# Kernel tuning notes

Measured on AMD Instinct MI355X. Metric: run time of the kernel, lower is better.

## Reference

```python
import jax, jax.numpy as jnp
import numpy as np

B, V, C = 256, 50, 40
VOCAB, D, H, NH, T = 10000, 256, 256, 8, 1000


def setup_inputs():
    key = jax.random.key(0)
    ks = jax.random.split(key, 24)
    f = lambda k, shape, s=0.05: jax.random.normal(k, shape, jnp.float32) * s
    # nn.Embedding(vocab_size+1, d_model, padding_idx=-1): last row is the padding row (zeros)
    emb = f(ks[0], (VOCAB + 1, D), 0.1).at[VOCAB].set(0.0)
    return dict(
        input_seqs=jax.random.randint(ks[1], (B, V, C), 0, VOCAB),
        seq_time_step=jax.random.uniform(ks[2], (B, V), jnp.float32, 0.0, 365.0),
        diffusion_time_t=jax.random.randint(ks[3], (B,), 0, T),
        normal_noise=jax.random.normal(ks[4], (B, V, D), jnp.float32),
        predicted_noise=jax.random.normal(ks[5], (B, V, D), jnp.float32),
        emb=emb,
        betas=jnp.asarray(np.linspace(1e-4, 0.02, T, dtype=np.float32)),
        tl_w=f(ks[6], (64, 1), 0.5), tl_b=f(ks[7], (64,), 0.1),
        tu_w=f(ks[8], (D, 64)), tu_b=f(ks[9], (D,), 0.01),
        in_proj_w=f(ks[10], (3 * D, D)), in_proj_b=f(ks[11], (3 * D,), 0.01),
        out_proj_w=f(ks[12], (D, D)), out_proj_b=f(ks[13], (D,), 0.01),
        w_ih=f(ks[14], (4 * H, D)), w_hh=f(ks[15], (4 * H, H)),
        b_ih=f(ks[16], (4 * H,), 0.01), b_hh=f(ks[17], (4 * H,), 0.01),
        c1_w=f(ks[18], (4 * H, H)), c1_b=f(ks[19], (4 * H,), 0.01),
        c2_w=f(ks[20], (4 * H, 4 * H)), c2_b=f(ks[21], (4 * H,), 0.01),
        co_w=f(ks[22], (2, 4 * H)), co_b=f(ks[23], (2,), 0.01),
    )


def _mha(q, kv, wi, bi, wo, bo):
    # torch MultiheadAttention on 2-D inputs -> unbatched; 'sequence length' = batch dim B
    hd = D // NH
    qp = (q @ wi[:D].T + bi[:D]).reshape(-1, NH, hd)
    kp = (kv @ wi[D:2 * D].T + bi[D:2 * D]).reshape(-1, NH, hd)
    vp = (kv @ wi[2 * D:].T + bi[2 * D:]).reshape(-1, NH, hd)
    s = jnp.einsum('qhd,khd->hqk', qp, kp) * (hd ** -0.5)
    o = jnp.einsum('hqk,khd->qhd', jax.nn.softmax(s, -1), vp).reshape(-1, D)
    return o @ wo.T + bo


def _lstm_final(seq, w_ih, w_hh, b_ih, b_hh):
    # unbatched nn.LSTM over the batch axis (length B). The original's try-branch always
    # raises (seq_h squeezed to 1-D), so the zero-init except-branch runs every visit.
    xg = seq @ w_ih.T + (b_ih + b_hh)  # [B, 4H]
    def step(carry, x):
        h, c = carry
        i, fg, g, o = jnp.split(x + h @ w_hh.T, 4)
        c = jax.nn.sigmoid(fg) * c + jax.nn.sigmoid(i) * jnp.tanh(g)
        h = jax.nn.sigmoid(o) * jnp.tanh(c)
        return (h, c), None
    z = jnp.zeros((H,), seq.dtype)
    (h, _), _ = jax.lax.scan(step, (z, z), xg)
    return h  # [H]


def _classify(h, w1, b1, w2, b2, wo, bo):
    h = jax.nn.relu(h @ w1.T + b1)
    h = jax.nn.relu(h @ w2.T + b2)
    return jax.nn.softmax(h @ wo.T + bo, -1)


def reference(input_seqs, seq_time_step, diffusion_time_t, normal_noise, predicted_noise,
              emb, betas, tl_w, tl_b, tu_w, tu_b, in_proj_w, in_proj_b, out_proj_w,
              out_proj_b, w_ih, w_hh, b_ih, b_hh, c1_w, c1_b, c2_w, c2_b, co_w, co_b):
    tt = seq_time_step[..., None] / 180.0
    tenc = (1.0 - jnp.tanh((tt @ tl_w.T + tl_b) ** 2)) @ tu_w.T + tu_b  # [B,V,D]
    ve = jax.nn.relu(emb[input_seqs]).sum(-2) + tenc                     # [B,V,D]
    alpha = jnp.cumprod(1.0 - betas)[diffusion_time_t][:, None, None]
    ven = ve * jnp.sqrt(alpha) + normal_noise * jnp.sqrt(1.0 - alpha)
    gen1 = ve + (ven - predicted_noise)
    # gen2 recurrence: row i = MHA(row i-1, gen1[:,i], gen1[:,i]); row -1 is the
    # vocab_size-filled initial tensor (valid negative index, try never fails).
    def att_step(prev, kv):
        out = _mha(prev, kv, in_proj_w, in_proj_b, out_proj_w, out_proj_b)
        return out, out
    _, gen2 = jax.lax.scan(att_step, jnp.full((B, D), float(VOCAB), ve.dtype),
                           gen1.transpose(1, 0, 2))                    # [V,B,D]
    lstm = lambda s: _lstm_final(s, w_ih, w_hh, b_ih, b_hh)
    hv = jax.vmap(lstm)(ve.transpose(1, 0, 2))  # [V,H]
    hg = jax.vmap(lstm)(gen2)                   # [V,H]
    res = jnp.broadcast_to(_classify(hv, c1_w, c1_b, c2_w, c2_b, co_w, co_b)[None], (B, V, 2))
    resg = jnp.broadcast_to(_classify(hg, c1_w, c1_b, c2_w, c2_b, co_w, co_b)[None], (B, V, 2))
    return (res, resg, res[:, -1], resg[:, -1], normal_noise, predicted_noise)
```

## Files before the change

### kernel.cpp

```cpp
#include <hip/hip_runtime.h>

#define BB 256
#define VV 50
#define CC 40
#define DD 256
#define HH 256
#define NHH 8
#define TT 1000

typedef unsigned short u16;
typedef unsigned int u32;
typedef _Float16 h2v __attribute__((ext_vector_type(2)));

__device__ __forceinline__ float blf(u16 x){ union{u32 u; float f;} z; z.u=(u32)x<<16; return z.f; }
__device__ __forceinline__ float ld(const void* p, long i, int f){
  if(f) return ((const float*)p)[i];
  return blf(((const u16*)p)[i]);
}
__device__ __forceinline__ u32 packh2(float a, float b){
  union { h2v h; u32 u; } z;
  z.h = h2v{(_Float16)a, (_Float16)b};
  return z.u;
}
__device__ __forceinline__ float fdot2(u32 a, u32 b, float c){
#if __has_builtin(__builtin_amdgcn_fdot2)
  union { u32 u; h2v h; } x, y; x.u=a; y.u=b;
  return __builtin_amdgcn_fdot2(x.h, y.h, c, false);
#else
  union { u32 u; _Float16 h[2]; } x, y; x.u=a; y.u=b;
  return c + (float)x.h[0]*(float)y.h[0] + (float)x.h[1]*(float)y.h[1];
#endif
}
__device__ __forceinline__ float sigm(float x){ return 1.f/(1.f+__expf(-x)); }
__device__ __forceinline__ float tanh_fast(float x){ return 1.f - 2.f/(__expf(2.f*x)+1.f); }

__global__ void k_flag(const void* betas, int* flag){
  if(threadIdx.x==0) flag[0] = (((const u32*)betas)[0] == 0x38D1B717u) ? 1 : 0;
}

__global__ void k_prep(const void* betas, const int* fl, float* sqa, float* s1a){
  __shared__ float sp[256];
  int t = threadIdx.x;
  int f = fl[0];
  float om[4]; float p = 1.f;
  #pragma unroll
  for(int k=0;k<4;k++){ int i=t*4+k; float be=(i<TT)?ld(betas,i,f):0.f; om[k]=1.f-be; p*=om[k]; }
  sp[t]=p; __syncthreads();
  for(int off=1; off<256; off<<=1){
    float x = (t>=off) ? sp[t-off]*sp[t] : sp[t];
    __syncthreads(); sp[t]=x; __syncthreads();
  }
  float c = (t>0)? sp[t-1] : 1.f;
  #pragma unroll
  for(int k=0;k<4;k++){
    c *= om[k]; int i=t*4+k;
    if(i<TT){ sqa[i]=sqrtf(c); s1a[i]=sqrtf(fmaxf(1.f-c,0.f)); }
  }
}

__global__ void k_packT(const void* src, float* dst, int N, int K, long elemoff, const int* fl){
  int i = blockIdx.x*256 + threadIdx.x;
  int tot = N*(K>>2);
  if(i>=tot) return;
  int f = fl[0];
  int d4 = i / N, j = i - d4*N;
  long o = elemoff + (long)j*K + (d4<<2);
  float4 r; r.x=ld(src,o,f); r.y=ld(src,o+1,f); r.z=ld(src,o+2,f); r.w=ld(src,o+3,f);
  ((float4*)dst)[i] = r;
}

__global__ void k_packQO(const void* src, u32* dst, long elemoff, const int* fl){
  int i = blockIdx.x*256 + threadIdx.x;
  if(i >= 32768) return;
  int f = fl[0];
  int c2 = i >> 8, j = i & 255;
  float a = ld(src, elemoff + (long)j*256 + 2*c2,     f);
  float b = ld(src, elemoff + (long)j*256 + 2*c2 + 1, f);
  dst[(c2>>2)*1024 + j*4 + (c2&3)] = packh2(a,b);
}

__global__ void k_packH(const void* src, u32* dst, int N, int K, const int* fl){
  int i = blockIdx.x*256 + threadIdx.x;
  int tot = N*(K>>1);
  if(i >= tot) return;
  int f = fl[0];
  int c2 = i / N, j = i - c2*N;
  float a = ld(src, (long)j*K + 2*c2,     f);
  float b = ld(src, (long)j*K + 2*c2 + 1, f);
  dst[(c2>>2)*(N*4) + j*4 + (c2&3)] = packh2(a,b);
}

__global__ void k_packW2(const void* src, u32* whhR, u32* wclQ, const int* fl){
  int i = blockIdx.x*256 + threadIdx.x;
  if(i >= 131072) return;
  int f = fl[0];
  int row = i >> 7, cp = i & 127;
  float a = ld(src, (long)row*256 + 2*cp,     f);
  float b = ld(src, (long)row*256 + 2*cp + 1, f);
  u32 v = packh2(a,b);
  int q = cp >> 5, pp = cp & 31;
  int rb = row & 127, m = row >> 7;
  int j = q*128 + rb;
  if(pp < 24){
    int idx = m*24 + pp;
    whhR[(idx>>2)*2048 + j*4 + (idx&3)] = v;
  } else {
    int h = (pp-24) >> 2, e = (pp-24) & 3;
    wclQ[((m*2+h)*512 + j)*4 + e] = v;
  }
}

__global__ void k_ve_gen1(const int* seqs, const void* sts, const int* dt,
    const void* nn, const void* pn, const void* emb, const void* tl_w, const void* tl_b,
    const float* tu4, const void* tu_b, const float* sqa, const float* s1a, const int* fl,
    float* ve, float* gen1){
  int bv = blockIdx.x; int b = bv / VV;
  int t = threadIdx.x;
  int f = fl[0];
  __shared__ float4 f4[16];
  __shared__ int idx[CC];
  float tt = ld(sts,bv,f) * (1.f/180.f);
  if(t<64){ float x = tt*ld(tl_w,t,f) + ld(tl_b,t,f); ((float*)f4)[t] = 1.f - tanhf(x*x); }
  if(t<CC) idx[t] = seqs[bv*CC+t];
  __syncthreads();
  float acc = ld(tu_b,t,f);
  const float4* tu = (const float4*)tu4;
  #pragma unroll
  for(int d4=0; d4<16; d4++){
    float4 w = tu[d4*DD + t];
    float4 fv = f4[d4];
    acc += fv.x*w.x+fv.y*w.y+fv.z*w.z+fv.w*w.w;
  }
  float s=0.f;
  for(int c=0;c<CC;c++){ float e = ld(emb,(long)idx[c]*DD + t,f); s += fmaxf(e,0.f); }
  float vev = s + acc;
  ve[bv*DD+t] = vev;
  int tb = dt[b];
  float sa=sqa[tb], s1=s1a[tb];
  gen1[bv*DD+t] = vev*(1.f+sa) + ld(nn,(long)bv*DD+t,f)*s1 - ld(pn,(long)bv*DD+t,f);
}

__global__ void k_copy(const void* nn, const void* pn, const int* fl, float* out){
  int i = blockIdx.x*256 + threadIdx.x;
  int f = fl[0];
  const int n = BB*VV*DD;
  if(i<n){ out[52224+i]=ld(nn,i,f); out[52224+n+i]=ld(pn,i,f); }
}

__global__ void k_kvproj(const float* gen1, const u32* wkP, const u32* wvP,
                         const void* bi, const int* fl, u32* kpHq, u32* vp){
  int g = blockIdx.x; int v = g>>4; int b0 = (g&15)<<4;
  int t = threadIdx.x;
  int f = fl[0];
  __shared__ __align__(16) u32 xp[16][128];
  for(int r=0;r<16;r++){
    float xv = gen1[((b0+r)*VV + v)*DD + t];
    float xb = __shfl_xor(xv, 1, 64);
    if((t&1)==0) xp[r][t>>1] = packh2(xv, xb);
  }
  __syncthreads();
  float ak[16], av[16];
  float bk = ld(bi,DD+t,f), bvv = ld(bi,2*DD+t,f);
  #pragma unroll
  for(int r=0;r<16;r++){ ak[r]=bk; av[r]=bvv; }
  const uint4* wk4 = (const uint4*)wkP;
  const uint4* wv4 = (const uint4*)wvP;
  for(int c8=0;c8<32;c8++){
    uint4 kk = wk4[c8*256+t], vv = wv4[c8*256+t];
    #pragma unroll
    for(int r=0;r<16;r++){
      uint4 xx = ((const uint4*)xp[r])[c8];
      ak[r] = fdot2(xx.x, kk.x, ak[r]); ak[r] = fdot2(xx.y, kk.y, ak[r]);
      ak[r] = fdot2(xx.z, kk.z, ak[r]); ak[r] = fdot2(xx.w, kk.w, ak[r]);
      av[r] = fdot2(xx.x, vv.x, av[r]); av[r] = fdot2(xx.y, vv.y, av[r]);
      av[r] = fdot2(xx.z, vv.z, av[r]); av[r] = fdot2(xx.w, vv.w, av[r]);
    }
  }
  #pragma unroll
  for(int r=0;r<16;r++){
    float a2 = __shfl_xor(ak[r], 1, 64);
    if((t&1)==0)
      kpHq[(size_t)v*32768 + (t>>3)*1024 + (size_t)(b0+r)*4 + ((t>>1)&3)] = packh2(ak[r], a2);
  }
  #pragma unroll
  for(int i2=0;i2<8;i2++){
    int k2 = (b0>>1) + i2;
    vp[(size_t)v*32768 + (k2>>2)*1024 + t*4 + (k2&3)] = packh2(av[2*i2], av[2*i2+1]);
  }
}

__global__ __launch_bounds__(256) void k_mha_all(const u32* kpHq, const u32* vp,
    const u32* wqp, const u32* wop, const void* ipb, const void* opb, const int* fl,
    float* gen2){
  int i = blockIdx.x, t = threadIdx.x;
  int f = fl[0];
  __shared__ __align__(16) u32 kls[32768];
  __shared__ __align__(16) u32 xp[128];
  __shared__ __align__(16) u32 qpp[128];
  __shared__ float s[NHH][257];
  __shared__ __align__(16) u32 sp[NHH][128];
  __shared__ __align__(16) u32 op[128];
  __shared__ float mh[NHH], rs[NHH];
  float bq = ld(ipb, t, f);
  float bo = ld(opb, t, f);
  if(t < 128) xp[t] = packh2(10000.f, 10000.f);
  __syncthreads();
  const uint4* xp4 = (const uint4*)xp;
  const uint4* op4 = (const uint4*)op;
  const uint4* wq4p = (const uint4*)wqp;
  const uint4* wo4p = (const uint4*)wop;
  const uint4* kls4 = (const uint4*)kls;
  const uint4* qp4  = (const uint4*)qpp;
  int hg = t>>5, ln = t&31;
  for(int v=0; v<VV; v++){
    {
      const u32* kg = kpHq + (size_t)v*32768;
#if __has_builtin(__builtin_amdgcn_global_load_lds)
      #pragma unroll
      for(int j=0;j<32;j++){
        __builtin_amdgcn_global_load_lds(
          (const __attribute__((address_space(1))) u32*)(kg + (j*256 + t)*4),
          (__attribute__((address_space(3))) u32*)(kls + (j*256 + t)*4), 16, 0, 0);
      }
#else
      const uint4* kg4 = (const uint4*)kg;
      uint4* kl4 = (uint4*)kls;
      #pragma unroll 8
      for(int j=0;j<32;j++) kl4[j*256+t] = kg4[j*256+t];
#endif
    }
    {
      float acc = bq;
      #pragma unroll 8
      for(int c8=0;c8<32;c8++){
        uint4 xx = xp4[c8];
        uint4 ww = wq4p[c8*256 + t];
        acc = fdot2(xx.x, ww.x, acc); acc = fdot2(xx.y, ww.y, acc);
        acc = fdot2(xx.z, ww.z, acc); acc = fdot2(xx.w, ww.w, acc);
      }
      float aq2 = __shfl_xor(acc, 1, 64);
      if((t&1)==0) qpp[t>>1] = packh2(acc, aq2);
    }
    asm volatile("s_waitcnt vmcnt(0)" ::: "memory");
    __syncthreads();
    {
      #pragma unroll
      for(int h=0; h<NHH; h++){
        float acc = 0.f;
        #pragma unroll
        for(int dd=0; dd<4; dd++){
          uint4 kk = kls4[(h*4+dd)*256 + t];
          uint4 qq = qp4[h*4+dd];
          acc = fdot2(qq.x, kk.x, acc); acc = fdot2(qq.y, kk.y, acc);
          acc = fdot2(qq.z, kk.z, acc); acc = fdot2(qq.w, kk.w, acc);
        }
        s[h][t] = acc*0.1767766952966369f;
      }
    }
    __syncthreads();
    float m=-3.0e38f;
    for(int k=ln;k<BB;k+=32) m=fmaxf(m, s[hg][k]);
    for(int off=16;off;off>>=1) m=fmaxf(m, __shfl_down(m,off,32));
    if(ln==0) mh[hg]=m;
    __syncthreads();
    #pragma unroll
    for(int h=0;h<NHH;h++) s[h][t]=__expf(s[h][t]-mh[h]);
    __syncthreads();
    float sm=0.f;
    for(int k=ln;k<BB;k+=32) sm += s[hg][k];
    for(int off=16;off;off>>=1) sm += __shfl_down(sm,off,32);
    if(ln==0) rs[hg]=1.f/sm;
    #pragma unroll
    for(int m2=t; m2<1024; m2+=256){
      int h = m2>>7, k2 = m2&127;
      sp[h][k2] = packh2(s[h][2*k2], s[h][2*k2+1]);
    }
    __syncthreads();
    {
      const uint4* vb = (const uint4*)(vp + (size_t)v*32768);
      const uint4* spv = (const uint4*)sp[hg];
      float acc = 0.f;
      #pragma unroll 8
      for(int k8=0;k8<32;k8++){
        uint4 pv = spv[k8];
        uint4 vv = vb[k8*256 + t];
        acc = fdot2(pv.x, vv.x, acc); acc = fdot2(pv.y, vv.y, acc);
        acc = fdot2(pv.z, vv.z, acc); acc = fdot2(pv.w, vv.w, acc);
      }
      float o = acc * rs[hg];
      float oo = __shfl_xor(o, 1, 64);
      if((t&1)==0) op[t>>1] = packh2(o, oo);
    }
    __syncthreads();
    {
      float acc = bo;
      #pragma unroll 8
      for(int c8=0;c8<32;c8++){
        uint4 xx = op4[c8];
        uint4 ww = wo4p[c8*256 + t];
        acc = fdot2(xx.x, ww.x, acc); acc = fdot2(xx.y, ww.y, acc);
        acc = fdot2(xx.z, ww.z, acc); acc = fdot2(xx.w, ww.w, acc);
      }
      gen2[((size_t)v*BB+i)*DD + t] = acc;
      float ax = __shfl_xor(acc, 1, 64);
      if((t&1)==0) xp[t>>1] = packh2(acc, ax);
    }
    __syncthreads();
  }
}

__global__ __launch_bounds__(256, 2) void k_xg(const float* inp, int is_ve, const u32* wihP,
                     const void* b_ih, const void* b_hh, const int* fl, u16* xg){
  int g = blockIdx.x; int v=g>>4; int b0=(g&15)<<4;
  int t = threadIdx.x;
  int f = fl[0];
  __shared__ __align__(16) u32 xp[16][128];
  for(int r=0;r<16;r++){
    int b = b0+r;
    const float* src = is_ve ? (inp + (b*VV+v)*DD) : (inp + (v*BB+b)*DD);
    float xv = src[t];
    float xb = __shfl_xor(xv, 1, 64);
    if((t&1)==0) xp[r][t>>1] = packh2(xv, xb);
  }
  __syncthreads();
  float acc[4][16];
  #pragma unroll
  for(int js=0;js<4;js++){
    float bsum = ld(b_ih,js*256+t,f) + ld(b_hh,js*256+t,f);
    #pragma unroll
    for(int r=0;r<16;r++) acc[js][r]=bsum;
  }
  const uint4* wp4 = (const uint4*)wihP;
  for(int c8=0; c8<32; c8++){
    uint4 w[4];
    #pragma unroll
    for(int js=0;js<4;js++) w[js] = wp4[c8*1024 + js*256 + t];
    #pragma unroll
    for(int r=0;r<16;r++){
      uint4 xx = ((const uint4*)xp[r])[c8];
      #pragma unroll
      for(int js=0;js<4;js++){
        acc[js][r] = fdot2(xx.x, w[js].x, acc[js][r]);
        acc[js][r] = fdot2(xx.y, w[js].y, acc[js][r]);
        acc[js][r] = fdot2(xx.z, w[js].z, acc[js][r]);
        acc[js][r] = fdot2(xx.w, w[js].w, acc[js][r]);
      }
    }
  }
  for(int r=0;r<16;r++)
    #pragma unroll
    for(int js=0;js<4;js++){
      union { _Float16 h; u16 u; } z;
      z.h = (_Float16)acc[js][r];
      xg[(size_t)(v*BB + b0 + r)*1024 + js*256 + t] = z.u;
    }
}

__global__ __attribute__((amdgpu_flat_work_group_size(512,512)))
__attribute__((amdgpu_waves_per_eu(2,2)))
void k_lstm3(const u16* xgA, const u16* xgB,
    const u32* whhR, const u32* wclQ, float* hfin){
  int b = blockIdx.x, j = threadIdx.x;
  int q = j >> 7, rb = j & 127;
  const u16* xgv = (b < VV) ? (xgA + (size_t)b*BB*1024) : (xgB + (size_t)(b-VV)*BB*1024);
  __shared__ __align__(16) u32 wcl[32768];
  __shared__ __align__(16) float pacc[4][1024];
  __shared__ __align__(16) u32 hp[128];
  u32 w[192];
  { const uint4* wr4 = (const uint4*)whhR;
    #pragma unroll
    for(int i4=0;i4<48;i4++){
      uint4 v = wr4[i4*512 + j];
      w[i4*4+0]=v.x; w[i4*4+1]=v.y; w[i4*4+2]=v.z; w[i4*4+3]=v.w;
    } }
  {
    const uint4* src = (const uint4*)wclQ;
    uint4* dst = (uint4*)wcl;
    #pragma unroll
    for(int i=0;i<16;i++) dst[i*512 + j] = src[i*512 + j];
  }
  if(j < 128) hp[j] = 0u;
  float c0 = 0.f, h_t = 0.f;
  __syncthreads();
  const uint4* hp4 = (const uint4*)hp;
  const uint4* wcl4 = (const uint4*)wcl;
  for(int s=0; s<BB; s++){
    asm volatile("" ::: "memory");
    u16 nx0=0,nx1=0,nx2=0,nx3=0;
    if(j < 256){
      nx0 = xgv[s*1024 +       j];
      nx1 = xgv[s*1024 + 256 + j];
      nx2 = xgv[s*1024 + 512 + j];
      nx3 = xgv[s*1024 + 768 + j];
    }
    float acc[8];
    #pragma unroll
    for(int m=0;m<8;m++) acc[m]=0.f;
    #pragma unroll
    for(int i=0;i<6;i++){
      uint4 hh = hp4[q*8 + i];
      #pragma unroll
      for(int m=0;m<8;m++){
        acc[m] = fdot2(hh.x, w[m*24 + i*4+0], acc[m]);
        acc[m] = fdot2(hh.y, w[m*24 + i*4+1], acc[m]);
        acc[m] = fdot2(hh.z, w[m*24 + i*4+2], acc[m]);
        acc[m] = fdot2(hh.w, w[m*24 + i*4+3], acc[m]);
      }
    }
    #pragma unroll
    for(int h=0;h<2;h++){
      uint4 hh = hp4[q*8 + 6 + h];
      #pragma unroll
      for(int m=0;m<8;m++){
        uint4 s4 = wcl4[(m*2+h)*512 + j];
        acc[m] = fdot2(hh.x, s4.x, acc[m]);
        acc[m] = fdot2(hh.y, s4.y, acc[m]);
        acc[m] = fdot2(hh.z, s4.z, acc[m]);
        acc[m] = fdot2(hh.w, s4.w, acc[m]);
      }
    }
    #pragma unroll
    for(int m=0;m<8;m++) pacc[q][m*128 + rb] = acc[m];
    __syncthreads();
    if(j < 256){
      float a0 = pacc[0][      j] + pacc[1][      j] + pacc[2][      j] + pacc[3][      j];
      float a1 = pacc[0][256 + j] + pacc[1][256 + j] + pacc[2][256 + j] + pacc[3][256 + j];
      float a2 = pacc[0][512 + j] + pacc[1][512 + j] + pacc[2][512 + j] + pacc[3][512 + j];
      float a3 = pacc[0][768 + j] + pacc[1][768 + j] + pacc[2][768 + j] + pacc[3][768 + j];
      float ai = a0 + (float)(*(const _Float16*)&nx0);
      float af = a1 + (float)(*(const _Float16*)&nx1);
      float ag = a2 + (float)(*(const _Float16*)&nx2);
      float ao = a3 + (float)(*(const _Float16*)&nx3);
      float ig = sigm(ai), fg = sigm(af), og = sigm(ao);
      float gg = tanh_fast(ag);
      c0 = fg*c0 + ig*gg;
      h_t = og*tanh_fast(c0);
      float ho = __shfl_xor(h_t, 1, 64);
      if((j&1)==0) hp[j>>1] = packh2(h_t, ho);
    }
    __syncthreads();
  }
  if(j < 256) hfin[b*HH + j] = h_t;
}

__global__ void k_cls(const float* hfin, const u32* c1p, const void* c1b,
                      const u32* c2p, const void* c2b, const void* cow, const void* cob,
                      const int* fl, float* cls){
  int blk = blockIdx.x;
  int t = threadIdx.x;
  int f = fl[0];
  __shared__ __align__(16) u32 hp1[128];
  __shared__ __align__(16) u32 h2p[512];
  __shared__ float h24[1024];
  __shared__ float red0[4], red1[4];
  {
    float hv = hfin[blk*HH + t];
    float hb = __shfl_xor(hv, 1, 64);
    if((t&1)==0) hp1[t>>1] = packh2(hv, hb);
  }
  __syncthreads();
  const uint4* hp14 = (const uint4*)hp1;
  const uint4* c1p4 = (const uint4*)c1p;
  {
    float a[4];
    #pragma unroll
    for(int js=0;js<4;js++) a[js]=ld(c1b,js*256+t,f);
    #pragma unroll 8
    for(int c8=0;c8<32;c8++){
      uint4 hh = hp14[c8];
      #pragma unroll
      for(int js=0;js<4;js++){
        uint4 ww = c1p4[c8*1024 + js*256+t];
        a[js] = fdot2(hh.x, ww.x, a[js]); a[js] = fdot2(hh.y, ww.y, a[js]);
        a[js] = fdot2(hh.z, ww.z, a[js]); a[js] = fdot2(hh.w, ww.w, a[js]);
      }
    }
    #pragma unroll
    for(int js=0;js<4;js++){
      float v = fmaxf(a[js],0.f);
      float vb = __shfl_xor(v, 1, 64);
      if((t&1)==0) h2p[(js*256+t)>>1] = packh2(v, vb);
    }
  }
  __syncthreads();
  const uint4* h2p4 = (const uint4*)h2p;
  const uint4* c2p4 = (const uint4*)c2p;
  {
    float a[4];
    #pragma unroll
    for(int js=0;js<4;js++) a[js]=ld(c2b,js*256+t,f);
    #pragma unroll 8
    for(int c8=0;c8<128;c8++){
      uint4 hh = h2p4[c8];
      #pragma unroll
      for(int js=0;js<4;js++){
        uint4 ww = c2p4[c8*1024 + js*256+t];
        a[js] = fdot2(hh.x, ww.x, a[js]); a[js] = fdot2(hh.y, ww.y, a[js]);
        a[js] = fdot2(hh.z, ww.z, a[js]); a[js] = fdot2(hh.w, ww.w, a[js]);
      }
    }
    #pragma unroll
    for(int js=0;js<4;js++) h24[js*256+t] = fmaxf(a[js],0.f);
  }
  __syncthreads();
  float p0=0.f,p1=0.f;
  #pragma unroll
  for(int js=0;js<4;js++){
    int j=js*256+t;
    float hv=h24[j];
    p0 += hv*ld(cow,j,f);
    p1 += hv*ld(cow,1024+j,f);
  }
  for(int off=32;off;off>>=1){ p0+=__shfl_down(p0,off,64); p1+=__shfl_down(p1,off,64); }
  if((t&63)==0){ red0[t>>6]=p0; red1[t>>6]=p1; }
  __syncthreads();
  if(t==0){
    float l0 = ld(cob,0,f) + red0[0]+red0[1]+red0[2]+red0[3];
    float l1 = ld(cob,1,f) + red1[0]+red1[1]+red1[2]+red1[3];
    float mm = fmaxf(l0,l1);
    float e0=__expf(l0-mm), e1=__expf(l1-mm);
    float inv = 1.f/(e0+e1);
    cls[blk*2] = e0*inv; cls[blk*2+1] = e1*inv;
  }
}

__global__ void k_out(const float* cls, float* out){
  int i = blockIdx.x*256 + threadIdx.x;
  if(i < BB*VV*2){
    int v = (i>>1) % VV, k = i&1;
    out[i] = cls[v*2+k];
    out[BB*VV*2 + i] = cls[(VV+v)*2+k];
  }
  if(i < BB*2){
    int k=i&1;
    out[2*BB*VV*2 + i]        = cls[(VV-1)*2+k];
    out[2*BB*VV*2 + BB*2 + i] = cls[(2*VV-1)*2+k];
  }
}

extern "C" void kernel_launch(void* const* d_in, const int* in_sizes, int n_in,
                              void* d_out, int out_size, void* d_ws, size_t ws_size,
                              hipStream_t stream){
  const int* seqs = (const int*)d_in[0];
  const void* sts  = d_in[1];
  const int* dt   = (const int*)d_in[2];
  const void* nn   = d_in[3];
  const void* pn   = d_in[4];
  const void* emb  = d_in[5];
  const void* betas= d_in[6];
  const void* tl_w = d_in[7];
  const void* tl_b = d_in[8];
  const void* tu_w = d_in[9];
  const void* tu_b = d_in[10];
  const void* ipw  = d_in[11];
  const void* ipb  = d_in[12];
  const void* opw  = d_in[13];
  const void* opb  = d_in[14];
  const void* wih  = d_in[15];
  const void* whh  = d_in[16];
  const void* bih  = d_in[17];
  const void* bhh  = d_in[18];
  const void* c1w  = d_in[19];
  const void* c1b  = d_in[20];
  const void* c2w  = d_in[21];
  const void* c2b  = d_in[22];
  const void* cow  = d_in[23];
  const void* cob  = d_in[24];

  char* base = (char*)d_ws;
  u32*   wkP  = (u32*)(base + 0);
  u32*   wvP  = (u32*)(base + 131072);
  u32*   wqp  = (u32*)(base + 524288);
  u32*   wop  = (u32*)(base + 655360);
  u32*   wihP = (u32*)(base + 786432);
  u32*   whhR = (u32*)(base + 1835008);
  u32*   wclQ = (u32*)(base + 2228224);
  u32*   c1p  = (u32*)(base + 2359296);
  u32*   c2p  = (u32*)(base + 3407872);
  float* tu4  = (float*)(base + 7602176);
  float* sqa  = (float*)(base + 7667712);
  float* s1a  = (float*)(base + 7671808);
  float* hfin = (float*)(base + 7675904);
  float* cls  = (float*)(base + 7778304);
  int*   flag = (int*)(base + 7779328);
  float* ve   = (float*)(base + 7783424);
  float* g12  = (float*)(base + 20890624);
  char*  arena= base + 33997824;
  u32*   kpHq = (u32*)(arena);
  u32*   vp   = (u32*)(arena + 13107200);
  u16*   xgA  = (u16*)(arena);
  u16*   xgB  = (u16*)(arena + 26214400);
  float* out  = (float*)d_out;

  k_flag<<<1,64,0,stream>>>(betas, flag);
  k_prep<<<1,256,0,stream>>>(betas, flag, sqa, s1a);
  k_packQO<<<128,256,0,stream>>>(ipw, wkP, 65536L,  flag);
  k_packQO<<<128,256,0,stream>>>(ipw, wvP, 131072L, flag);
  k_packQO<<<128,256,0,stream>>>(ipw, wqp, 0, flag);
  k_packQO<<<128,256,0,stream>>>(opw, wop, 0, flag);
  k_packH<<<512,256,0,stream>>>(wih, wihP, 1024, 256, flag);
  k_packW2<<<512,256,0,stream>>>(whh, whhR, wclQ, flag);
  k_packH<<<512,256,0,stream>>>(c1w, c1p, 1024, 256, flag);
  k_packH<<<2048,256,0,stream>>>(c2w, c2p, 1024, 1024, flag);
  k_packT<<<16,256,0,stream>>>(tu_w, tu4, 256, 64, 0, flag);

  k_ve_gen1<<<BB*VV,256,0,stream>>>(seqs,sts,dt,nn,pn,emb,tl_w,tl_b,tu4,tu_b,sqa,s1a,flag,ve,g12);
  k_copy<<<(BB*VV*DD+255)/256,256,0,stream>>>(nn,pn,flag,out);

  k_kvproj<<<VV*16,256,0,stream>>>(g12, wkP, wvP, ipb, flag, kpHq, vp);
  k_mha_all<<<BB,256,0,stream>>>(kpHq, vp, wqp, wop, ipb, opb, flag, g12);

  k_xg<<<VV*16,256,0,stream>>>(ve,  1, wihP, bih, bhh, flag, xgA);
  k_xg<<<VV*16,256,0,stream>>>(g12, 0, wihP, bih, bhh, flag, xgB);
  k_lstm3<<<100,512,0,stream>>>(xgA, xgB, whhR, wclQ, hfin);

  k_cls<<<2*VV,256,0,stream>>>(hfin, c1p, c1b, c2p, c2b, cow, cob, flag, cls);
  k_out<<<100,256,0,stream>>>(cls, out);
}
```

Measured before the change: 1.563 ms.

## Fuse weight-pack kernels into one launch and use shuffle reductions in LSTM

All the flag, prep and weight-packing kernels are merged into a single mega-kernel that dispatches on block index, so eleven small launches become one. The LSTM recurrence is restructured so that each wave owns 16 hidden rows across the four K-quarters. Partial sums are then reduced with cross-lane shuffles instead of a shared-memory pacc array and a second barrier. The hidden state is double-buffered so only one __syncthreads per timestep remains, and the whh packing layout is changed to match the new thread mapping.

```diff
diff --git a/kernel.cpp b/kernel.cpp
--- a/kernel.cpp
+++ b/kernel.cpp
@@ -34,14 +34,9 @@
 __device__ __forceinline__ float sigm(float x){ return 1.f/(1.f+__expf(-x)); }
 __device__ __forceinline__ float tanh_fast(float x){ return 1.f - 2.f/(__expf(2.f*x)+1.f); }
 
-__global__ void k_flag(const void* betas, int* flag){
-  if(threadIdx.x==0) flag[0] = (((const u32*)betas)[0] == 0x38D1B717u) ? 1 : 0;
-}
-
-__global__ void k_prep(const void* betas, const int* fl, float* sqa, float* s1a){
-  __shared__ float sp[256];
-  int t = threadIdx.x;
-  int f = fl[0];
+
+__device__ __forceinline__ void prep_body(const void* betas, int f, int t,
+                                          float* sqa, float* s1a, float* sp){
   float om[4]; float p = 1.f;
   #pragma unroll
   for(int k=0;k<4;k++){ int i=t*4+k; float be=(i<TT)?ld(betas,i,f):0.f; om[k]=1.f-be; p*=om[k]; }
@@ -58,49 +53,50 @@
   }
 }
 
-__global__ void k_packT(const void* src, float* dst, int N, int K, long elemoff, const int* fl){
-  int i = blockIdx.x*256 + threadIdx.x;
-  int tot = N*(K>>2);
-  if(i>=tot) return;
-  int f = fl[0];
-  int d4 = i / N, j = i - d4*N;
-  long o = elemoff + (long)j*K + (d4<<2);
-  float4 r; r.x=ld(src,o,f); r.y=ld(src,o+1,f); r.z=ld(src,o+2,f); r.w=ld(src,o+3,f);
-  ((float4*)dst)[i] = r;
-}
-
-__global__ void k_packQO(const void* src, u32* dst, long elemoff, const int* fl){
-  int i = blockIdx.x*256 + threadIdx.x;
+__device__ __forceinline__ void packQO_body(const void* src, u32* dst, long elemoff,
+                                            int f, int lb, int t){
+  int i = lb*256 + t;
   if(i >= 32768) return;
-  int f = fl[0];
   int c2 = i >> 8, j = i & 255;
   float a = ld(src, elemoff + (long)j*256 + 2*c2,     f);
   float b = ld(src, elemoff + (long)j*256 + 2*c2 + 1, f);
   dst[(c2>>2)*1024 + j*4 + (c2&3)] = packh2(a,b);
 }
 
-__global__ void k_packH(const void* src, u32* dst, int N, int K, const int* fl){
-  int i = blockIdx.x*256 + threadIdx.x;
+__device__ __forceinline__ void packH_body(const void* src, u32* dst, int N, int K,
+                                           int f, int lb, int t){
+  int i = lb*256 + t;
   int tot = N*(K>>1);
   if(i >= tot) return;
-  int f = fl[0];
   int c2 = i / N, j = i - c2*N;
   float a = ld(src, (long)j*K + 2*c2,     f);
   float b = ld(src, (long)j*K + 2*c2 + 1, f);
   dst[(c2>>2)*(N*4) + j*4 + (c2&3)] = packh2(a,b);
 }
 
-__global__ void k_packW2(const void* src, u32* whhR, u32* wclQ, const int* fl){
-  int i = blockIdx.x*256 + threadIdx.x;
+__device__ __forceinline__ void packT_body(const void* src, float* dst, int N, int K,
+                                           int f, int lb, int t){
+  int i = lb*256 + t;
+  int tot = N*(K>>2);
+  if(i>=tot) return;
+  int d4 = i / N, j = i - d4*N;
+  long o = (long)j*K + (d4<<2);
+  float4 r; r.x=ld(src,o,f); r.y=ld(src,o+1,f); r.z=ld(src,o+2,f); r.w=ld(src,o+3,f);
+  ((float4*)dst)[i] = r;
+}
+
+__device__ __forceinline__ void packW2_body(const void* src, u32* whhR, u32* wclQ,
+                                            int f, int lb, int t){
+  int i = lb*256 + t;
   if(i >= 131072) return;
-  int f = fl[0];
   int row = i >> 7, cp = i & 127;
   float a = ld(src, (long)row*256 + 2*cp,     f);
   float b = ld(src, (long)row*256 + 2*cp + 1, f);
   u32 v = packh2(a,b);
   int q = cp >> 5, pp = cp & 31;
-  int rb = row & 127, m = row >> 7;
-  int j = q*128 + rb;
+  int m = row >> 7, rsB = row & 127;
+  int w = rsB >> 4, li = rsB & 15;
+  int j = w*64 + q*16 + li;
   if(pp < 24){
     int idx = m*24 + pp;
     whhR[(idx>>2)*2048 + j*4 + (idx&3)] = v;
@@ -108,6 +104,29 @@
     int h = (pp-24) >> 2, e = (pp-24) & 3;
     wclQ[((m*2+h)*512 + j)*4 + e] = v;
   }
+}
+
+__global__ void k_mega(const void* betas, const void* ipw, const void* opw,
+    const void* wih, const void* whh, const void* c1w, const void* c2w, const void* tu_w,
+    int* flag, float* sqa, float* s1a,
+    u32* wkP, u32* wvP, u32* wqp, u32* wop, u32* wihP,
+    u32* whhR, u32* wclQ, u32* c1p, u32* c2p, float* tu4){
+  __shared__ float sp[256];
+  int f = (((const u32*)betas)[0] == 0x38D1B717u) ? 1 : 0;
+  int g = blockIdx.x, t = threadIdx.x;
+  if(g == 0){
+    if(t == 0) flag[0] = f;
+    prep_body(betas, f, t, sqa, s1a, sp);
+  }
+  else if(g < 129)  packQO_body(ipw, wkP, 65536L,  f, g-1,   t);
+  else if(g < 257)  packQO_body(ipw, wvP, 131072L, f, g-129, t);
+  else if(g < 385)  packQO_body(ipw, wqp, 0L,      f, g-257, t);
+  else if(g < 513)  packQO_body(opw, wop, 0L,      f, g-385, t);
+  else if(g < 1025) packH_body(wih, wihP, 1024, 256,  f, g-513,  t);
+  else if(g < 1537) packW2_body(whh, whhR, wclQ,      f, g-1025, t);
+  else if(g < 2049) packH_body(c1w, c1p, 1024, 256,   f, g-1537, t);
+  else if(g < 4097) packH_body(c2w, c2p, 1024, 1024,  f, g-2049, t);
+  else              packT_body(tu_w, tu4, 256, 64,    f, g-4097, t);
 }
 
 __global__ void k_ve_gen1(const int* seqs, const void* sts, const int* dt,
@@ -361,11 +380,12 @@
 void k_lstm3(const u16* xgA, const u16* xgB,
     const u32* whhR, const u32* wclQ, float* hfin){
   int b = blockIdx.x, j = threadIdx.x;
-  int q = j >> 7, rb = j & 127;
+  int l = j & 63;
+  int q = l >> 4, li = l & 15;
+  int rs = (j>>6)*16 + li;
   const u16* xgv = (b < VV) ? (xgA + (size_t)b*BB*1024) : (xgB + (size_t)(b-VV)*BB*1024);
   __shared__ __align__(16) u32 wcl[32768];
-  __shared__ __align__(16) float pacc[4][1024];
-  __shared__ __align__(16) u32 hp[128];
+  __shared__ __align__(16) u32 hp[2][128];
   u32 w[192];
   { const uint4* wr4 = (const uint4*)whhR;
     #pragma unroll
@@ -379,26 +399,22 @@
     #pragma unroll
     for(int i=0;i<16;i++) dst[i*512 + j] = src[i*512 + j];
   }
-  if(j < 128) hp[j] = 0u;
-  float c0 = 0.f, h_t = 0.f;
-  __syncthreads();
-  const uint4* hp4 = (const uint4*)hp;
+  if(j < 128) hp[0][j] = 0u;
+  float cA = 0.f, cB = 0.f, hA = 0.f, hB = 0.f;
+  __syncthreads();
   const uint4* wcl4 = (const uint4*)wcl;
   for(int s=0; s<BB; s++){
     asm volatile("" ::: "memory");
-    u16 nx0=0,nx1=0,nx2=0,nx3=0;
-    if(j < 256){
-      nx0 = xgv[s*1024 +       j];
-      nx1 = xgv[s*1024 + 256 + j];
-      nx2 = xgv[s*1024 + 512 + j];
-      nx3 = xgv[s*1024 + 768 + j];
-    }
+    const uint4* hc = (const uint4*)hp[s&1];
+    u16 nx[8];
+    #pragma unroll
+    for(int m=0;m<8;m++) nx[m] = xgv[s*1024 + rs + 128*m];
     float acc[8];
     #pragma unroll
     for(int m=0;m<8;m++) acc[m]=0.f;
     #pragma unroll
     for(int i=0;i<6;i++){
-      uint4 hh = hp4[q*8 + i];
+      uint4 hh = hc[q*8 + i];
       #pragma unroll
       for(int m=0;m<8;m++){
         acc[m] = fdot2(hh.x, w[m*24 + i*4+0], acc[m]);
@@ -409,7 +425,7 @@
     }
     #pragma unroll
     for(int h=0;h<2;h++){
-      uint4 hh = hp4[q*8 + 6 + h];
+      uint4 hh = hc[q*8 + 6 + h];
       #pragma unroll
       for(int m=0;m<8;m++){
         uint4 s4 = wcl4[(m*2+h)*512 + j];
@@ -420,27 +436,35 @@
       }
     }
     #pragma unroll
-    for(int m=0;m<8;m++) pacc[q][m*128 + rb] = acc[m];
-    __syncthreads();
-    if(j < 256){
-      float a0 = pacc[0][      j] + pacc[1][      j] + pacc[2][      j] + pacc[3][      j];
-      float a1 = pacc[0][256 + j] + pacc[1][256 + j] + pacc[2][256 + j] + pacc[3][256 + j];
-      float a2 = pacc[0][512 + j] + pacc[1][512 + j] + pacc[2][512 + j] + pacc[3][512 + j];
-      float a3 = pacc[0][768 + j] + pacc[1][768 + j] + pacc[2][768 + j] + pacc[3][768 + j];
-      float ai = a0 + (float)(*(const _Float16*)&nx0);
-      float af = a1 + (float)(*(const _Float16*)&nx1);
-      float ag = a2 + (float)(*(const _Float16*)&nx2);
-      float ao = a3 + (float)(*(const _Float16*)&nx3);
-      float ig = sigm(ai), fg = sigm(af), og = sigm(ao);
-      float gg = tanh_fast(ag);
-      c0 = fg*c0 + ig*gg;
-      h_t = og*tanh_fast(c0);
-      float ho = __shfl_xor(h_t, 1, 64);
-      if((j&1)==0) hp[j>>1] = packh2(h_t, ho);
-    }
-    __syncthreads();
-  }
-  if(j < 256) hfin[b*HH + j] = h_t;
+    for(int m=0;m<8;m++){
+      float a = acc[m];
+      a += __shfl_xor(a, 16, 64);
+      a += __shfl_xor(a, 32, 64);
+      acc[m] = a + (float)(*(const _Float16*)&nx[m]);
+    }
+    {
+      float igA=sigm(acc[0]), fgA=sigm(acc[2]), ogA=sigm(acc[6]);
+      float ggA=tanh_fast(acc[4]);
+      cA = fgA*cA + igA*ggA;
+      hA = ogA*tanh_fast(cA);
+      float igB=sigm(acc[1]), fgB=sigm(acc[3]), ogB=sigm(acc[7]);
+      float ggB=tanh_fast(acc[5]);
+      cB = fgB*cB + igB*ggB;
+      hB = ogB*tanh_fast(cB);
+      float hA2 = __shfl_xor(hA, 1, 64);
+      float hB2 = __shfl_xor(hB, 1, 64);
+      if(q==0 && (li&1)==0){
+        int base = (j>>6)*8 + (li>>1);
+        hp[(s+1)&1][base]      = packh2(hA, hA2);
+        hp[(s+1)&1][64 + base] = packh2(hB, hB2);
+      }
+    }
+    __syncthreads();
+  }
+  if(q==0){
+    hfin[b*HH + rs]       = hA;
+    hfin[b*HH + rs + 128] = hB;
+  }
 }
 
 __global__ void k_cls(const float* hfin, const u32* c1p, const void* c1b,
@@ -592,17 +616,8 @@
   u16*   xgB  = (u16*)(arena + 26214400);
   float* out  = (float*)d_out;
 
-  k_flag<<<1,64,0,stream>>>(betas, flag);
-  k_prep<<<1,256,0,stream>>>(betas, flag, sqa, s1a);
-  k_packQO<<<128,256,0,stream>>>(ipw, wkP, 65536L,  flag);
-  k_packQO<<<128,256,0,stream>>>(ipw, wvP, 131072L, flag);
-  k_packQO<<<128,256,0,stream>>>(ipw, wqp, 0, flag);
-  k_packQO<<<128,256,0,stream>>>(opw, wop, 0, flag);
-  k_packH<<<512,256,0,stream>>>(wih, wihP, 1024, 256, flag);
-  k_packW2<<<512,256,0,stream>>>(whh, whhR, wclQ, flag);
-  k_packH<<<512,256,0,stream>>>(c1w, c1p, 1024, 256, flag);
-  k_packH<<<2048,256,0,stream>>>(c2w, c2p, 1024, 1024, flag);
-  k_packT<<<16,256,0,stream>>>(tu_w, tu4, 256, 64, 0, flag);
+  k_mega<<<4113,256,0,stream>>>(betas, ipw, opw, wih, whh, c1w, c2w, tu_w,
+      flag, sqa, s1a, wkP, wvP, wqp, wop, wihP, whhR, wclQ, c1p, c2p, tu4);
 
   k_ve_gen1<<<BB*VV,256,0,stream>>>(seqs,sts,dt,nn,pn,emb,tl_w,tl_b,tu4,tu_b,sqa,s1a,flag,ve,g12);
   k_copy<<<(BB*VV*DD+255)/256,256,0,stream>>>(nn,pn,flag,out);
```

After: 1.672 ms. 1.07x slower.
